# Kernel optimization log

Measured on AMD Instinct MI355X. Metric: run time of the kernel, lower is better.

## Reference

```python
import jax, jax.numpy as jnp
import numpy as np

B, S, H, E, T, L = 128, 1024, 512, 512, 64, 128


def setup_inputs() -> dict:
    key = jax.random.key(0)
    ks = jax.random.split(key, 20)
    s = 0.02
    inp = {
        "sent_lengths": jax.random.randint(ks[0], (B,), 1, S, dtype=jnp.int32),
        "output_length": T,
        "decoder_input": jax.random.normal(ks[1], (B, E), jnp.float32),
        "h0": jax.random.normal(ks[2], (B, H), jnp.float32),
        "c0": jax.random.normal(ks[3], (B, H), jnp.float32),
        "context": jax.random.normal(ks[4], (B, S, H), jnp.float32),
        "cur_labels": jax.random.randint(ks[5], (B, T), 0, L, dtype=jnp.int32),
        "cur_max_nsymbs": jax.random.randint(ks[6], (B,), 0, 10, dtype=jnp.int32),
        # parameters
        "label_emb": jax.random.normal(ks[7], (L, E), jnp.float32) * s,
        "W_ih": jax.random.normal(ks[8], (4 * H, E), jnp.float32) * s,
        "b_ih": jnp.zeros((4 * H,), jnp.float32),
        "W_hh": jax.random.normal(ks[9], (4 * H, H), jnp.float32) * s,
        "b_hh": jnp.zeros((4 * H,), jnp.float32),
        "W_ho": jax.random.normal(ks[10], (H, 2 * H), jnp.float32) * s,
        "b_ho": jnp.zeros((H,), jnp.float32),
        "W_attn_in": jax.random.normal(ks[11], (H, H), jnp.float32) * s,
        "b_attn_in": jnp.zeros((H,), jnp.float32),
        "W_attn_ctx": jax.random.normal(ks[12], (H, H), jnp.float32) * s,
        "b_attn_ctx": jnp.zeros((H,), jnp.float32),
        "V": jax.random.uniform(ks[13], (H,), jnp.float32, -1.0, 1.0),
        "W_out": jax.random.normal(ks[14], (L, 2 * H + E), jnp.float32) * s,
        "b_out": jnp.zeros((L,), jnp.float32),
    }
    # padding_idx row of the label embedding is zero (torch nn.Embedding semantics)
    inp["label_emb"] = inp["label_emb"].at[0].set(0.0)
    return inp


def _decode(output_length, decoder_input, h0, c0, context, cur_labels,
            label_emb, W_ih, b_ih, W_hh, b_hh, W_ho, b_ho,
            W_attn_in, b_attn_in, W_attn_ctx, b_attn_ctx, V, W_out, b_out):
    # Precompute the 1x1-conv context projection once (identical math to per-step conv).
    ctx = jnp.einsum("bsh,gh->bsg", context, W_attn_ctx) + b_attn_ctx  # [B,S,H]

    # Teacher-forced input sequence: x_0 = decoder_input, x_i = emb(labels[:, i-1]).
    emb = label_emb[cur_labels]                     # [B,T,E]
    xs = jnp.concatenate(
        [decoder_input[None], jnp.swapaxes(emb, 0, 1)[: output_length - 1]], axis=0
    )                                               # [T,B,E]

    def step(carry, x):
        h, c = carry
        gates = x @ W_ih.T + b_ih + h @ W_hh.T + b_hh          # [B,4H]
        i_g, f_g, g_g, o_g = jnp.split(gates, 4, axis=1)
        c_t = jax.nn.sigmoid(f_g) * c + jax.nn.sigmoid(i_g) * jnp.tanh(g_g)
        h_lstm = jax.nn.sigmoid(o_g) * jnp.tanh(c_t)            # [B,H]
        # pointer attention
        inp = h_lstm @ W_attn_in.T + b_attn_in                  # [B,H]
        att = jnp.einsum("bsh,h->bs", jnp.tanh(inp[:, None, :] + ctx), V)
        alpha = jax.nn.softmax(att, axis=-1)                    # [B,S]
        weighted = jnp.einsum("bs,bsh->bh", alpha, ctx)         # [B,H]
        hidden_t = jnp.tanh(jnp.concatenate([weighted, h_lstm], 1) @ W_ho.T + b_ho)
        out = jnp.concatenate([hidden_t, weighted, x], 1) @ W_out.T + b_out  # [B,L]
        return (hidden_t, c_t), out

    (h_f, c_f), outs = jax.lax.scan(step, (h0, c0), xs)  # outs [T,B,L]
    outputs = jnp.transpose(outs, (1, 0, 2))             # [B,T,L]
    preds = jnp.argmax(outputs, axis=-1)                 # [B,T]
    return outputs, preds, h_f, c_f


def reference(sent_lengths, output_length, decoder_input, h0, c0, context,
              cur_labels, cur_max_nsymbs, label_emb, W_ih, b_ih, W_hh, b_hh,
              W_ho, b_ho, W_attn_in, b_attn_in, W_attn_ctx, b_attn_ctx, V,
              W_out, b_out):
    # cur_batch_len = len(sent_lengths) == B, so hidden slicing is a no-op here.
    # cur_max_nsymbs unused (constrained_decoding=None path).
    return _decode(output_length, decoder_input, h0, c0, context, cur_labels,
                   label_emb, W_ih, b_ih, W_hh, b_hh, W_ho, b_ho,
                   W_attn_in, b_attn_in, W_attn_ctx, b_attn_ctx, V, W_out, b_out)
```

## Files before the change

kernel.cpp:

```cpp
#include <hip/hip_runtime.h>
#include <hip/hip_bf16.h>
#include <math.h>

#define B_ 128
#define S_ 1024
#define H_ 512
#define E_ 512
#define T_ 64
#define L_ 128
#define G4H 2048
#define QS 8

typedef __attribute__((ext_vector_type(8))) short bf16x8;
typedef __attribute__((ext_vector_type(4))) float f32x4;

__device__ inline float sigmoidf_(float x) { return 1.f / (1.f + expf(-x)); }
__device__ inline float fast_tanhf_(float x) {
    float e = __expf(2.f * x);
    return 1.f - 2.f / (e + 1.f);
}
__device__ inline unsigned f2bf1(float f) {
    unsigned u = __float_as_uint(f);
    return (u + 0x7fffu + ((u >> 16) & 1u)) >> 16;
}

#define LDP 40
__global__ __launch_bounds__(256) void gemm_split(
    const float* __restrict__ A, int lda,
    const float* __restrict__ W, int ldw,
    const float* __restrict__ bias,
    const float* __restrict__ Cinit, int ldci,
    float* __restrict__ C, int ldc,
    int K, int act, int perm)
{
    __shared__ unsigned short Ah[128 * LDP];
    __shared__ unsigned short Al[128 * LDP];
    __shared__ unsigned short Bh[128 * LDP];
    __shared__ unsigned short Bl[128 * LDP];
    const int n0 = blockIdx.x * 128;
    const int m0 = blockIdx.y * 128;
    const int t = threadIdx.x;
    const int lane = t & 63, wv = t >> 6;
    const int wr = wv >> 1, wc = wv & 1;
    const int row = t >> 1, koff = (t & 1) * 16;

    f32x4 acc[4][4] = {};

    float av[16], wvv[16];
    {
        const float* ap = A + (size_t)(m0 + row) * lda + koff;
        const float* wp = W + (size_t)(n0 + row) * ldw + koff;
#pragma unroll
        for (int q = 0; q < 4; ++q) {
            *reinterpret_cast<float4*>(&av[q * 4]) = *reinterpret_cast<const float4*>(ap + q * 4);
            *reinterpret_cast<float4*>(&wvv[q * 4]) = *reinterpret_cast<const float4*>(wp + q * 4);
        }
    }

    for (int kt = 0; kt < K; kt += 32) {
        unsigned short ah[16], al[16], bh[16], bl[16];
#pragma unroll
        for (int e = 0; e < 16; ++e) {
            unsigned ha = f2bf1(av[e]);
            float hf = __uint_as_float(ha << 16);
            ah[e] = (unsigned short)ha;
            al[e] = (unsigned short)f2bf1(av[e] - hf);
            unsigned hw = f2bf1(wvv[e]);
            float hwf = __uint_as_float(hw << 16);
            bh[e] = (unsigned short)hw;
            bl[e] = (unsigned short)f2bf1(wvv[e] - hwf);
        }
        __syncthreads();
        *reinterpret_cast<uint4*>(&Ah[row * LDP + koff])     = *reinterpret_cast<uint4*>(&ah[0]);
        *reinterpret_cast<uint4*>(&Ah[row * LDP + koff + 8]) = *reinterpret_cast<uint4*>(&ah[8]);
        *reinterpret_cast<uint4*>(&Al[row * LDP + koff])     = *reinterpret_cast<uint4*>(&al[0]);
        *reinterpret_cast<uint4*>(&Al[row * LDP + koff + 8]) = *reinterpret_cast<uint4*>(&al[8]);
        *reinterpret_cast<uint4*>(&Bh[row * LDP + koff])     = *reinterpret_cast<uint4*>(&bh[0]);
        *reinterpret_cast<uint4*>(&Bh[row * LDP + koff + 8]) = *reinterpret_cast<uint4*>(&bh[8]);
        *reinterpret_cast<uint4*>(&Bl[row * LDP + koff])     = *reinterpret_cast<uint4*>(&bl[0]);
        *reinterpret_cast<uint4*>(&Bl[row * LDP + koff + 8]) = *reinterpret_cast<uint4*>(&bl[8]);
        __syncthreads();

        if (kt + 32 < K) {
            const float* ap = A + (size_t)(m0 + row) * lda + kt + 32 + koff;
            const float* wp = W + (size_t)(n0 + row) * ldw + kt + 32 + koff;
#pragma unroll
            for (int q = 0; q < 4; ++q) {
                *reinterpret_cast<float4*>(&av[q * 4]) = *reinterpret_cast<const float4*>(ap + q * 4);
                *reinterpret_cast<float4*>(&wvv[q * 4]) = *reinterpret_cast<const float4*>(wp + q * 4);
            }
        }

        bf16x8 fah[4], fal[4], fbh[4], fbl[4];
        const int kq = (lane >> 4) * 8;
#pragma unroll
        for (int i = 0; i < 4; ++i) {
            const int ar = wr * 64 + i * 16 + (lane & 15);
            const int br = wc * 64 + i * 16 + (lane & 15);
            fah[i] = *reinterpret_cast<const bf16x8*>(&Ah[ar * LDP + kq]);
            fal[i] = *reinterpret_cast<const bf16x8*>(&Al[ar * LDP + kq]);
            fbh[i] = *reinterpret_cast<const bf16x8*>(&Bh[br * LDP + kq]);
            fbl[i] = *reinterpret_cast<const bf16x8*>(&Bl[br * LDP + kq]);
        }
#pragma unroll
        for (int i = 0; i < 4; ++i)
#pragma unroll
            for (int j = 0; j < 4; ++j) {
                acc[i][j] = __builtin_amdgcn_mfma_f32_16x16x32_bf16(fah[i], fbh[j], acc[i][j], 0, 0, 0);
                acc[i][j] = __builtin_amdgcn_mfma_f32_16x16x32_bf16(fal[i], fbh[j], acc[i][j], 0, 0, 0);
                acc[i][j] = __builtin_amdgcn_mfma_f32_16x16x32_bf16(fah[i], fbl[j], acc[i][j], 0, 0, 0);
            }
    }

#pragma unroll
    for (int i = 0; i < 4; ++i)
#pragma unroll
        for (int j = 0; j < 4; ++j) {
            const int n = n0 + wc * 64 + j * 16 + (lane & 15);
            const float bs = bias ? bias[n] : 0.f;
#pragma unroll
            for (int r = 0; r < 4; ++r) {
                const int m = m0 + wr * 64 + i * 16 + (lane >> 4) * 4 + r;
                float v = acc[i][j][r] + bs;
                if (Cinit) v += Cinit[(size_t)m * ldci + n];
                if (act == 1) v = tanhf(v);
                size_t crow;
                if (perm) { int bb = m & 127, tt = m >> 7; crow = ((size_t)bb * T_ + tt) * ldc; }
                else crow = (size_t)m * ldc;
                C[crow + n] = v;
            }
        }
}

__global__ __launch_bounds__(128) void k_perm(
    const float* __restrict__ W_ih, const float* __restrict__ W_hh,
    const float* __restrict__ b_ih, const float* __restrict__ b_hh,
    float* __restrict__ Wip, float* __restrict__ Whp, float* __restrict__ bp)
{
    int rp = blockIdx.x;
    int h = rp >> 2, g = rp & 3;
    int src = g * 512 + h;
    int t = threadIdx.x;
    const float4* si = reinterpret_cast<const float4*>(W_ih + (size_t)src * 512);
    const float4* sh = reinterpret_cast<const float4*>(W_hh + (size_t)src * 512);
    float4* di = reinterpret_cast<float4*>(Wip + (size_t)rp * 512);
    float4* dh = reinterpret_cast<float4*>(Whp + (size_t)rp * 512);
    di[t] = si[t];
    dh[t] = sh[t];
    if (t == 0) bp[rp] = b_ih[src] + b_hh[src];
}

__global__ __launch_bounds__(256) void k_gateslstm(
    const float* __restrict__ hbuf,
    const float* __restrict__ Whp,
    const float* __restrict__ xproj_t,
    float* __restrict__ cbuf,
    float* __restrict__ hlstm)
{
    __shared__ float As[16][32];
    __shared__ float Ws[16][64];
    const int n0 = blockIdx.x * 64;
    const int m0 = blockIdx.y * 32;
    const int t = threadIdx.x;
    const int tx = t & 15;
    const int ty = t >> 4;
    const int alr = t >> 3, alk = (t & 7) * 2;
    const int wlr = t >> 2, wlk = (t & 3) * 4;

    float acc[2][4] = {};

    float2 pa = *reinterpret_cast<const float2*>(hbuf + (size_t)(m0 + alr) * 512 + alk);
    float4 pv = *reinterpret_cast<const float4*>(Whp + (size_t)(n0 + wlr) * 512 + wlk);

    for (int k0 = 0; k0 < 512; k0 += 16) {
        __syncthreads();
        As[alk + 0][alr] = pa.x; As[alk + 1][alr] = pa.y;
        Ws[wlk + 0][wlr] = pv.x; Ws[wlk + 1][wlr] = pv.y;
        Ws[wlk + 2][wlr] = pv.z; Ws[wlk + 3][wlr] = pv.w;
        __syncthreads();
        if (k0 + 16 < 512) {
            pa = *reinterpret_cast<const float2*>(hbuf + (size_t)(m0 + alr) * 512 + k0 + 16 + alk);
            pv = *reinterpret_cast<const float4*>(Whp + (size_t)(n0 + wlr) * 512 + k0 + 16 + wlk);
        }
#pragma unroll
        for (int kk = 0; kk < 16; ++kk) {
            float a[2], b[4];
            a[0] = As[kk][ty * 2]; a[1] = As[kk][ty * 2 + 1];
#pragma unroll
            for (int j = 0; j < 4; ++j) b[j] = Ws[kk][tx * 4 + j];
#pragma unroll
            for (int i = 0; i < 2; ++i)
#pragma unroll
                for (int j = 0; j < 4; ++j) acc[i][j] = fmaf(a[i], b[j], acc[i][j]);
        }
    }

    const int h = (n0 >> 2) + tx;
#pragma unroll
    for (int i = 0; i < 2; ++i) {
        const int b = m0 + ty * 2 + i;
        float4 xp = *reinterpret_cast<const float4*>(xproj_t + (size_t)b * G4H + n0 + tx * 4);
        float ig = sigmoidf_(acc[i][0] + xp.x);
        float fg = sigmoidf_(acc[i][1] + xp.y);
        float gg = tanhf(acc[i][2] + xp.z);
        float og = sigmoidf_(acc[i][3] + xp.w);
        float c = fg * cbuf[(size_t)b * 512 + h] + ig * gg;
        cbuf[(size_t)b * 512 + h] = c;
        hlstm[(size_t)b * 512 + h] = og * tanhf(c);
    }
}

__global__ __launch_bounds__(256) void gemm_stepk(
    const float* __restrict__ A, int lda,
    const float* __restrict__ W, int ldw,
    float* __restrict__ P, int N, int Kc)
{
    __shared__ float As[16][128];
    __shared__ float Ws[16][64];
    const int n0 = blockIdx.x * 64;
    const int k0 = blockIdx.y * Kc;
    const int t = threadIdx.x;
    const int tx = t & 15;
    const int ty = t >> 4;
    const int ar = t >> 1, akq = (t & 1) * 8;
    const int wr = t >> 2, wkq = (t & 3) * 4;

    float acc[8][4] = {};

    float4 a0 = *reinterpret_cast<const float4*>(A + (size_t)ar * lda + k0 + akq);
    float4 a1 = *reinterpret_cast<const float4*>(A + (size_t)ar * lda + k0 + akq + 4);
    float4 w0 = *reinterpret_cast<const float4*>(W + (size_t)(n0 + wr) * ldw + k0 + wkq);

    for (int kb = 0; kb < Kc; kb += 16) {
        __syncthreads();
        As[akq + 0][ar] = a0.x; As[akq + 1][ar] = a0.y; As[akq + 2][ar] = a0.z; As[akq + 3][ar] = a0.w;
        As[akq + 4][ar] = a1.x; As[akq + 5][ar] = a1.y; As[akq + 6][ar] = a1.z; As[akq + 7][ar] = a1.w;
        Ws[wkq + 0][wr] = w0.x; Ws[wkq + 1][wr] = w0.y; Ws[wkq + 2][wr] = w0.z; Ws[wkq + 3][wr] = w0.w;
        __syncthreads();
        if (kb + 16 < Kc) {
            a0 = *reinterpret_cast<const float4*>(A + (size_t)ar * lda + k0 + kb + 16 + akq);
            a1 = *reinterpret_cast<const float4*>(A + (size_t)ar * lda + k0 + kb + 16 + akq + 4);
            w0 = *reinterpret_cast<const float4*>(W + (size_t)(n0 + wr) * ldw + k0 + kb + 16 + wkq);
        }
#pragma unroll
        for (int kk = 0; kk < 16; ++kk) {
            float a[8], b[4];
#pragma unroll
            for (int i = 0; i < 8; ++i) a[i] = As[kk][ty * 8 + i];
#pragma unroll
            for (int j = 0; j < 4; ++j) b[j] = Ws[kk][tx * 4 + j];
#pragma unroll
            for (int i = 0; i < 8; ++i)
#pragma unroll
                for (int j = 0; j < 4; ++j) acc[i][j] = fmaf(a[i], b[j], acc[i][j]);
        }
    }

#pragma unroll
    for (int i = 0; i < 8; ++i) {
        const int m = ty * 8 + i;
#pragma unroll
        for (int j = 0; j < 4; ++j)
            P[((size_t)blockIdx.y * 128 + m) * N + n0 + tx * 4 + j] = acc[i][j];
    }
}

__global__ __launch_bounds__(256) void k_who(
    const float* __restrict__ pm, const float* __restrict__ pl,
    const float* __restrict__ pw, const float* __restrict__ hlstm,
    const float* __restrict__ W_ho,
    float* __restrict__ P, float* __restrict__ hist_t)
{
    __shared__ float As[16][128];
    __shared__ float Ws[16][64];
    __shared__ float eql[128][QS];
    const int n0 = blockIdx.x * 64;
    const int k0 = blockIdx.y * 128;
    const int t = threadIdx.x;
    const int tx = t & 15;
    const int ty = t >> 4;
    const int ar = t >> 1, akq = (t & 1) * 8;
    const int wr = t >> 2, wkq = (t & 3) * 4;
    const bool merge_side = (k0 < 512);
    const bool writer = (blockIdx.x == 0) && merge_side;

    if (merge_side && t < 128) {
        float mq[QS], eq[QS];
        float M = -INFINITY;
#pragma unroll
        for (int q = 0; q < QS; ++q) { mq[q] = pm[QS * t + q]; M = fmaxf(M, mq[q]); }
        float Lt = 0.f;
#pragma unroll
        for (int q = 0; q < QS; ++q) { eq[q] = __expf(mq[q] - M); Lt += eq[q] * pl[QS * t + q]; }
        float inv = 1.f / Lt;
#pragma unroll
        for (int q = 0; q < QS; ++q) eql[t][q] = eq[q] * inv;
    }
    __syncthreads();

    float acc[8][4] = {};
    float av[8];
    float4 w0;

    auto load_stage = [&](int kb) {
        const int kg = k0 + kb + akq;
        if (merge_side) {
#pragma unroll
            for (int e = 0; e < 8; ++e) av[e] = 0.f;
#pragma unroll
            for (int q = 0; q < QS; ++q) {
                const float* pr = pw + (size_t)(QS * ar + q) * 512 + kg;
                float4 pa = *reinterpret_cast<const float4*>(pr);
                float4 pb = *reinterpret_cast<const float4*>(pr + 4);
                float qw = eql[ar][q];
                av[0] = fmaf(qw, pa.x, av[0]); av[1] = fmaf(qw, pa.y, av[1]);
                av[2] = fmaf(qw, pa.z, av[2]); av[3] = fmaf(qw, pa.w, av[3]);
                av[4] = fmaf(qw, pb.x, av[4]); av[5] = fmaf(qw, pb.y, av[5]);
                av[6] = fmaf(qw, pb.z, av[6]); av[7] = fmaf(qw, pb.w, av[7]);
            }
            if (writer) {
                *reinterpret_cast<float4*>(hist_t + (size_t)ar * 1024 + 512 + kg) = *reinterpret_cast<float4*>(&av[0]);
                *reinterpret_cast<float4*>(hist_t + (size_t)ar * 1024 + 512 + kg + 4) = *reinterpret_cast<float4*>(&av[4]);
            }
        } else {
            *reinterpret_cast<float4*>(&av[0]) = *reinterpret_cast<const float4*>(hlstm + (size_t)ar * 512 + kg - 512);
            *reinterpret_cast<float4*>(&av[4]) = *reinterpret_cast<const float4*>(hlstm + (size_t)ar * 512 + kg - 512 + 4);
        }
        w0 = *reinterpret_cast<const float4*>(W_ho + (size_t)(n0 + wr) * 1024 + k0 + kb + wkq);
    };

    load_stage(0);

    for (int kb = 0; kb < 128; kb += 16) {
        __syncthreads();
        As[akq + 0][ar] = av[0]; As[akq + 1][ar] = av[1]; As[akq + 2][ar] = av[2]; As[akq + 3][ar] = av[3];
        As[akq + 4][ar] = av[4]; As[akq + 5][ar] = av[5]; As[akq + 6][ar] = av[6]; As[akq + 7][ar] = av[7];
        Ws[wkq + 0][wr] = w0.x; Ws[wkq + 1][wr] = w0.y; Ws[wkq + 2][wr] = w0.z; Ws[wkq + 3][wr] = w0.w;
        __syncthreads();
        if (kb + 16 < 128) load_stage(kb + 16);
#pragma unroll
        for (int kk = 0; kk < 16; ++kk) {
            float a[8], b[4];
#pragma unroll
            for (int i = 0; i < 8; ++i) a[i] = As[kk][ty * 8 + i];
#pragma unroll
            for (int j = 0; j < 4; ++j) b[j] = Ws[kk][tx * 4 + j];
#pragma unroll
            for (int i = 0; i < 8; ++i)
#pragma unroll
                for (int j = 0; j < 4; ++j) acc[i][j] = fmaf(a[i], b[j], acc[i][j]);
        }
    }

#pragma unroll
    for (int i = 0; i < 8; ++i) {
        const int m = ty * 8 + i;
#pragma unroll
        for (int j = 0; j < 4; ++j)
            P[((size_t)blockIdx.y * 128 + m) * 512 + n0 + tx * 4 + j] = acc[i][j];
    }
}

__global__ void k_embed(const float* __restrict__ dec_in, const int* __restrict__ labels,
                        const float* __restrict__ emb, float* __restrict__ X)
{
    size_t total = (size_t)T_ * B_ * E_;
    for (size_t i = (size_t)blockIdx.x * blockDim.x + threadIdx.x; i < total;
         i += (size_t)gridDim.x * blockDim.x) {
        int e = (int)(i % E_);
        int b = (int)((i / E_) % B_);
        int t = (int)(i / ((size_t)E_ * B_));
        float v;
        if (t == 0) v = dec_in[b * E_ + e];
        else {
            int lab = labels[b * T_ + (t - 1)];
            v = emb[(size_t)lab * E_ + e];
        }
        X[i] = v;
    }
}

__global__ void k_init(const float* __restrict__ h0, const float* __restrict__ c0,
                       float* __restrict__ hbuf, float* __restrict__ cbuf)
{
    int i = blockIdx.x * blockDim.x + threadIdx.x;
    hbuf[i] = h0[i];
    cbuf[i] = c0[i];
}

__global__ __launch_bounds__(512) void k_attn(const float* __restrict__ ctx,
    const float* __restrict__ Pa, const float* __restrict__ b_ain,
    const float* __restrict__ Vv,
    float* __restrict__ pm, float* __restrict__ pl, float* __restrict__ pw)
{
    int blk = blockIdx.x;
    int b = blk >> 3, q = blk & 7;
    int tid = threadIdx.x, lane = tid & 63, wv = tid >> 6;

    __shared__ float inp_sh[512];
    inp_sh[tid] = Pa[(size_t)b * 512 + tid]
                + Pa[(size_t)(128 + b) * 512 + tid]
                + Pa[(size_t)(256 + b) * 512 + tid]
                + Pa[(size_t)(384 + b) * 512 + tid]
                + b_ain[tid];
    __syncthreads();

    float inpr[8], vr[8];
    {
        const float4* v4 = reinterpret_cast<const float4*>(Vv) + lane * 2;
        *(float4*)&vr[0] = v4[0];   *(float4*)&vr[4] = v4[1];
#pragma unroll
        for (int k = 0; k < 8; ++k) inpr[k] = inp_sh[lane * 8 + k];
    }
    const float* sp = ctx + ((size_t)b * S_ + q * 128 + wv * 16) * H_ + lane * 8;

    float m = -INFINITY, l = 0.f, w[8] = {};
    float4 c0 = *reinterpret_cast<const float4*>(sp);
    float4 c1 = *reinterpret_cast<const float4*>(sp + 4);
    for (int si = 0; si < 16; ++si) {
        float4 u0 = c0, u1 = c1;
        if (si < 15) {
            c0 = *reinterpret_cast<const float4*>(sp + (size_t)(si + 1) * H_);
            c1 = *reinterpret_cast<const float4*>(sp + (size_t)(si + 1) * H_ + 4);
        }
        float c8[8];
        *(float4*)&c8[0] = u0; *(float4*)&c8[4] = u1;
        float t = 0.f;
#pragma unroll
        for (int k = 0; k < 8; ++k) t = fmaf(fast_tanhf_(inpr[k] + c8[k]), vr[k], t);
#pragma unroll
        for (int off = 32; off > 0; off >>= 1) t += __shfl_xor(t, off);
        float mn = fmaxf(m, t);
        float sc = __expf(m - mn);
        float p  = __expf(t - mn);
        l = l * sc + p;
#pragma unroll
        for (int k = 0; k < 8; ++k) w[k] = w[k] * sc + p * c8[k];
        m = mn;
    }

    __shared__ float wl[8 * 512];
    __shared__ float ml[8], ll[8];
#pragma unroll
    for (int k = 0; k < 8; ++k) wl[wv * 512 + lane * 8 + k] = w[k];
    if (lane == 0) { ml[wv] = m; ll[wv] = l; }
    __syncthreads();

    float M = ml[0];
#pragma unroll
    for (int u = 1; u < 8; ++u) M = fmaxf(M, ml[u]);
    float lt = 0.f, wt = 0.f;
#pragma unroll
    for (int u = 0; u < 8; ++u) {
        float e = __expf(ml[u] - M);
        lt += e * ll[u];
        wt += e * wl[u * 512 + tid];
    }
    if (tid == 0) { pm[blk] = M; pl[blk] = lt; }
    pw[(size_t)blk * 512 + tid] = wt;
}

__global__ __launch_bounds__(256) void k_whofin(const float* __restrict__ Po,
    const float* __restrict__ b_ho, float* __restrict__ hbuf, float* __restrict__ hist_t)
{
    int i = blockIdx.x * blockDim.x + threadIdx.x;
    int b = i >> 9, h = i & 511;
    float v = b_ho[h];
#pragma unroll
    for (int ks = 0; ks < 8; ++ks) v += Po[((size_t)ks * 128 + b) * 512 + h];
    v = tanhf(v);
    hbuf[i] = v;
    hist_t[(size_t)b * 1024 + h] = v;
}

__global__ __launch_bounds__(128) void k_argmax(const float* __restrict__ outp,
                                                float* __restrict__ preds)
{
    int row = blockIdx.x;
    int tid = threadIdx.x;
    float v = outp[(size_t)row * L_ + tid];
    int idx = tid;
#pragma unroll
    for (int off = 32; off > 0; off >>= 1) {
        float ov = __shfl_xor(v, off);
        int oi = __shfl_xor(idx, off);
        if (ov > v || (ov == v && oi < idx)) { v = ov; idx = oi; }
    }
    __shared__ float sv[2];
    __shared__ int si[2];
    if ((tid & 63) == 0) { sv[tid >> 6] = v; si[tid >> 6] = idx; }
    __syncthreads();
    if (tid == 0) {
        float v0 = sv[0], v1 = sv[1];
        int i0 = si[0], i1 = si[1];
        int r = (v1 > v0 || (v1 == v0 && i1 < i0)) ? i1 : i0;
        preds[row] = (float)r;
    }
}

__global__ void k_final(const float* __restrict__ hbuf, const float* __restrict__ cbuf,
                        float* __restrict__ hf, float* __restrict__ cf)
{
    int i = blockIdx.x * blockDim.x + threadIdx.x;
    hf[i] = hbuf[i];
    cf[i] = cbuf[i];
}

extern "C" void kernel_launch(void* const* d_in, const int* in_sizes, int n_in,
                              void* d_out, int out_size, void* d_ws, size_t ws_size,
                              hipStream_t stream)
{
    const float* dec_in  = (const float*)d_in[2];
    const float* h0      = (const float*)d_in[3];
    const float* c0      = (const float*)d_in[4];
    const float* context = (const float*)d_in[5];
    const int*   labels  = (const int*)d_in[6];
    const float* emb     = (const float*)d_in[8];
    const float* W_ih    = (const float*)d_in[9];
    const float* b_ih    = (const float*)d_in[10];
    const float* W_hh    = (const float*)d_in[11];
    const float* b_hh    = (const float*)d_in[12];
    const float* W_ho    = (const float*)d_in[13];
    const float* b_ho    = (const float*)d_in[14];
    const float* W_ain   = (const float*)d_in[15];
    const float* b_ain   = (const float*)d_in[16];
    const float* W_actx  = (const float*)d_in[17];
    const float* b_actx  = (const float*)d_in[18];
    const float* Vv      = (const float*)d_in[19];
    const float* W_out   = (const float*)d_in[20];
    const float* b_out   = (const float*)d_in[21];

    float* ws = (float*)d_ws;
    float* X     = ws; ws += (size_t)T_ * B_ * E_;
    float* xproj = ws; ws += (size_t)T_ * B_ * G4H;
    float* xout  = ws; ws += (size_t)T_ * B_ * L_;
    float* ctx   = ws; ws += (size_t)B_ * S_ * H_;
    float* hist  = ws; ws += (size_t)T_ * B_ * 1024;
    float* Wip   = ws; ws += (size_t)G4H * 512;
    float* Whp   = ws; ws += (size_t)G4H * 512;
    float* bp    = ws; ws += G4H;
    float* Pa    = ws; ws += (size_t)4 * B_ * H_;
    float* Po    = ws; ws += (size_t)8 * B_ * H_;
    float* cbuf  = ws; ws += (size_t)B_ * H_;
    float* hbuf  = ws; ws += (size_t)B_ * H_;
    float* hlstm = ws; ws += (size_t)B_ * H_;
    float* pm    = ws; ws += (size_t)B_ * QS;
    float* pl    = ws; ws += (size_t)B_ * QS;
    float* pw    = ws; ws += (size_t)B_ * QS * 512;

    float* out_logits = (float*)d_out;
    float* out_preds  = out_logits + (size_t)B_ * T_ * L_;
    float* out_hf     = out_preds + (size_t)B_ * T_;
    float* out_cf     = out_hf + (size_t)B_ * H_;

    k_embed<<<2048, 256, 0, stream>>>(dec_in, labels, emb, X);
    k_init<<<256, 256, 0, stream>>>(h0, c0, hbuf, cbuf);
    k_perm<<<G4H, 128, 0, stream>>>(W_ih, W_hh, b_ih, b_hh, Wip, Whp, bp);
    gemm_split<<<dim3(16, 64), 256, 0, stream>>>(X, E_, Wip, E_, bp, nullptr, 0,
                                                 xproj, G4H, E_, 0, 0);
    gemm_split<<<dim3(1, 64), 256, 0, stream>>>(X, E_, W_out + 1024, 1536, b_out, nullptr, 0,
                                                xout, L_, E_, 0, 0);
    gemm_split<<<dim3(4, 1024), 256, 0, stream>>>(context, H_, W_actx, H_, b_actx, nullptr, 0,
                                                  ctx, H_, H_, 0, 0);

    for (int t = 0; t < T_; ++t) {
        float* hist_t = hist + (size_t)t * B_ * 1024;
        k_gateslstm<<<dim3(32, 4), 256, 0, stream>>>(hbuf, Whp,
                                                     xproj + (size_t)t * B_ * G4H,
                                                     cbuf, hlstm);
        gemm_stepk<<<dim3(8, 4), 256, 0, stream>>>(hlstm, H_, W_ain, H_, Pa, H_, 128);
        k_attn<<<B_ * QS, 512, 0, stream>>>(ctx, Pa, b_ain, Vv, pm, pl, pw);
        k_who<<<dim3(8, 8), 256, 0, stream>>>(pm, pl, pw, hlstm, W_ho, Po, hist_t);
        k_whofin<<<256, 256, 0, stream>>>(Po, b_ho, hbuf, hist_t);
    }

    gemm_split<<<dim3(1, 64), 256, 0, stream>>>(hist, 1024, W_out, 1536, nullptr,
                                                xout, L_, out_logits, L_, 1024, 0, 1);
    k_argmax<<<B_ * T_, 128, 0, stream>>>(out_logits, out_preds);
    k_final<<<256, 256, 0, stream>>>(hbuf, cbuf, out_hf, out_cf);
}
```

Before: 7.470 ms.

## Fuse W_ho split-K GEMM with tanh finalize and deepen attention context prefetch

The split-K W_ho GEMM plus its separate reduce/tanh kernel are replaced by one kernel. Each block now covers a 16-row by 64-column tile over the full K=1024, computes the attention merge on the fly, and applies bias and tanh before writing hbuf and hist. This removes one launch per decode step and the Po partial-sum buffer. In exchange each block runs a longer serial K loop with two barriers per 16-wide slice and scalar gathers. The attention kernel also prefetches four context rows ahead instead of one, to hide global load latency.

After: 10.51 ms. +40.7%, slower.

```diff
diff --git a/kernel.cpp b/kernel.cpp
--- a/kernel.cpp
+++ b/kernel.cpp
@@ -265,102 +265,6 @@
     }
 }
 
-__global__ __launch_bounds__(256) void k_who(
-    const float* __restrict__ pm, const float* __restrict__ pl,
-    const float* __restrict__ pw, const float* __restrict__ hlstm,
-    const float* __restrict__ W_ho,
-    float* __restrict__ P, float* __restrict__ hist_t)
-{
-    __shared__ float As[16][128];
-    __shared__ float Ws[16][64];
-    __shared__ float eql[128][QS];
-    const int n0 = blockIdx.x * 64;
-    const int k0 = blockIdx.y * 128;
-    const int t = threadIdx.x;
-    const int tx = t & 15;
-    const int ty = t >> 4;
-    const int ar = t >> 1, akq = (t & 1) * 8;
-    const int wr = t >> 2, wkq = (t & 3) * 4;
-    const bool merge_side = (k0 < 512);
-    const bool writer = (blockIdx.x == 0) && merge_side;
-
-    if (merge_side && t < 128) {
-        float mq[QS], eq[QS];
-        float M = -INFINITY;
-#pragma unroll
-        for (int q = 0; q < QS; ++q) { mq[q] = pm[QS * t + q]; M = fmaxf(M, mq[q]); }
-        float Lt = 0.f;
-#pragma unroll
-        for (int q = 0; q < QS; ++q) { eq[q] = __expf(mq[q] - M); Lt += eq[q] * pl[QS * t + q]; }
-        float inv = 1.f / Lt;
-#pragma unroll
-        for (int q = 0; q < QS; ++q) eql[t][q] = eq[q] * inv;
-    }
-    __syncthreads();
-
-    float acc[8][4] = {};
-    float av[8];
-    float4 w0;
-
-    auto load_stage = [&](int kb) {
-        const int kg = k0 + kb + akq;
-        if (merge_side) {
-#pragma unroll
-            for (int e = 0; e < 8; ++e) av[e] = 0.f;
-#pragma unroll
-            for (int q = 0; q < QS; ++q) {
-                const float* pr = pw + (size_t)(QS * ar + q) * 512 + kg;
-                float4 pa = *reinterpret_cast<const float4*>(pr);
-                float4 pb = *reinterpret_cast<const float4*>(pr + 4);
-                float qw = eql[ar][q];
-                av[0] = fmaf(qw, pa.x, av[0]); av[1] = fmaf(qw, pa.y, av[1]);
-                av[2] = fmaf(qw, pa.z, av[2]); av[3] = fmaf(qw, pa.w, av[3]);
-                av[4] = fmaf(qw, pb.x, av[4]); av[5] = fmaf(qw, pb.y, av[5]);
-                av[6] = fmaf(qw, pb.z, av[6]); av[7] = fmaf(qw, pb.w, av[7]);
-            }
-            if (writer) {
-                *reinterpret_cast<float4*>(hist_t + (size_t)ar * 1024 + 512 + kg) = *reinterpret_cast<float4*>(&av[0]);
-                *reinterpret_cast<float4*>(hist_t + (size_t)ar * 1024 + 512 + kg + 4) = *reinterpret_cast<float4*>(&av[4]);
-            }
-        } else {
-            *reinterpret_cast<float4*>(&av[0]) = *reinterpret_cast<const float4*>(hlstm + (size_t)ar * 512 + kg - 512);
-            *reinterpret_cast<float4*>(&av[4]) = *reinterpret_cast<const float4*>(hlstm + (size_t)ar * 512 + kg - 512 + 4);
-        }
-        w0 = *reinterpret_cast<const float4*>(W_ho + (size_t)(n0 + wr) * 1024 + k0 + kb + wkq);
-    };
-
-    load_stage(0);
-
-    for (int kb = 0; kb < 128; kb += 16) {
-        __syncthreads();
-        As[akq + 0][ar] = av[0]; As[akq + 1][ar] = av[1]; As[akq + 2][ar] = av[2]; As[akq + 3][ar] = av[3];
-        As[akq + 4][ar] = av[4]; As[akq + 5][ar] = av[5]; As[akq + 6][ar] = av[6]; As[akq + 7][ar] = av[7];
-        Ws[wkq + 0][wr] = w0.x; Ws[wkq + 1][wr] = w0.y; Ws[wkq + 2][wr] = w0.z; Ws[wkq + 3][wr] = w0.w;
-        __syncthreads();
-        if (kb + 16 < 128) load_stage(kb + 16);
-#pragma unroll
-        for (int kk = 0; kk < 16; ++kk) {
-            float a[8], b[4];
-#pragma unroll
-            for (int i = 0; i < 8; ++i) a[i] = As[kk][ty * 8 + i];
-#pragma unroll
-            for (int j = 0; j < 4; ++j) b[j] = Ws[kk][tx * 4 + j];
-#pragma unroll
-            for (int i = 0; i < 8; ++i)
-#pragma unroll
-                for (int j = 0; j < 4; ++j) acc[i][j] = fmaf(a[i], b[j], acc[i][j]);
-        }
-    }
-
-#pragma unroll
-    for (int i = 0; i < 8; ++i) {
-        const int m = ty * 8 + i;
-#pragma unroll
-        for (int j = 0; j < 4; ++j)
-            P[((size_t)blockIdx.y * 128 + m) * 512 + n0 + tx * 4 + j] = acc[i][j];
-    }
-}
-
 __global__ void k_embed(const float* __restrict__ dec_in, const int* __restrict__ labels,
                         const float* __restrict__ emb, float* __restrict__ X)
 {
@@ -415,14 +319,8 @@
     const float* sp = ctx + ((size_t)b * S_ + q * 128 + wv * 16) * H_ + lane * 8;
 
     float m = -INFINITY, l = 0.f, w[8] = {};
-    float4 c0 = *reinterpret_cast<const float4*>(sp);
-    float4 c1 = *reinterpret_cast<const float4*>(sp + 4);
-    for (int si = 0; si < 16; ++si) {
-        float4 u0 = c0, u1 = c1;
-        if (si < 15) {
-            c0 = *reinterpret_cast<const float4*>(sp + (size_t)(si + 1) * H_);
-            c1 = *reinterpret_cast<const float4*>(sp + (size_t)(si + 1) * H_ + 4);
-        }
+
+    auto process = [&](float4 u0, float4 u1) {
         float c8[8];
         *(float4*)&c8[0] = u0; *(float4*)&c8[4] = u1;
         float t = 0.f;
@@ -437,6 +335,25 @@
 #pragma unroll
         for (int k = 0; k < 8; ++k) w[k] = w[k] * sc + p * c8[k];
         m = mn;
+    };
+
+    float4 a0[4], a1[4];
+#pragma unroll
+    for (int j = 0; j < 4; ++j) {
+        a0[j] = *reinterpret_cast<const float4*>(sp + (size_t)j * H_);
+        a1[j] = *reinterpret_cast<const float4*>(sp + (size_t)j * H_ + 4);
+    }
+    for (int so = 0; so < 16; so += 4) {
+        const bool pf = (so + 4 < 16);
+#pragma unroll
+        for (int j = 0; j < 4; ++j) {
+            float4 u0 = a0[j], u1 = a1[j];
+            if (pf) {
+                a0[j] = *reinterpret_cast<const float4*>(sp + (size_t)(so + 4 + j) * H_);
+                a1[j] = *reinterpret_cast<const float4*>(sp + (size_t)(so + 4 + j) * H_ + 4);
+            }
+            process(u0, u1);
+        }
     }
 
     __shared__ float wl[8 * 512];
@@ -460,17 +377,94 @@
     pw[(size_t)blk * 512 + tid] = wt;
 }
 
-__global__ __launch_bounds__(256) void k_whofin(const float* __restrict__ Po,
-    const float* __restrict__ b_ho, float* __restrict__ hbuf, float* __restrict__ hist_t)
+__global__ __launch_bounds__(256) void k_whoF(
+    const float* __restrict__ pm, const float* __restrict__ pl,
+    const float* __restrict__ pw, const float* __restrict__ hlstm,
+    const float* __restrict__ W_ho, const float* __restrict__ b_ho,
+    const float* __restrict__ cbuf,
+    float* __restrict__ hbuf, float* __restrict__ hist_t, int last)
+{
+    __shared__ float As[16][16];
+    __shared__ float Ws[16][64];
+    __shared__ float eql[16][QS];
+    const int n0 = blockIdx.x * 64;
+    const int m0 = blockIdx.y * 16;
+    const int nt = blockIdx.x;
+    const int t0 = threadIdx.x;
+    const int ty = t0 >> 4, tx = t0 & 15;
+    const int alr = t0 & 15, alk = t0 >> 4;
+    const int wlr = t0 & 63, wk4 = (t0 >> 6) * 4;
+
+    if (t0 < 16) {
+        const int row = m0 + t0;
+        float mq[QS], eq[QS];
+        float M = -INFINITY;
+#pragma unroll
+        for (int q = 0; q < QS; ++q) { mq[q] = pm[row * QS + q]; M = fmaxf(M, mq[q]); }
+        float Lt = 0.f;
+#pragma unroll
+        for (int q = 0; q < QS; ++q) { eq[q] = __expf(mq[q] - M); Lt += eq[q] * pl[row * QS + q]; }
+        float inv = 1.f / Lt;
+#pragma unroll
+        for (int q = 0; q < QS; ++q) eql[t0][q] = eq[q] * inv;
+    }
+    __syncthreads();
+
+    float acc[4] = {};
+    auto ld_a = [&](int k0) -> float {
+        const int row = m0 + alr;
+        const int k = k0 + alk;
+        if (k0 < 512) {
+            float v = 0.f;
+#pragma unroll
+            for (int q = 0; q < QS; ++q)
+                v = fmaf(eql[alr][q], pw[((size_t)(row * QS + q)) * 512 + k], v);
+            if (nt == 0) hist_t[(size_t)row * 1024 + 512 + k] = v;
+            return v;
+        }
+        return hlstm[(size_t)row * 512 + k - 512];
+    };
+
+    float pa = ld_a(0);
+    float4 pv = *reinterpret_cast<const float4*>(W_ho + (size_t)(n0 + wlr) * 1024 + wk4);
+    for (int k0 = 0; k0 < 1024; k0 += 16) {
+        __syncthreads();
+        As[alk][alr] = pa;
+        Ws[wk4 + 0][wlr] = pv.x; Ws[wk4 + 1][wlr] = pv.y;
+        Ws[wk4 + 2][wlr] = pv.z; Ws[wk4 + 3][wlr] = pv.w;
+        __syncthreads();
+        if (k0 + 16 < 1024) {
+            pa = ld_a(k0 + 16);
+            pv = *reinterpret_cast<const float4*>(W_ho + (size_t)(n0 + wlr) * 1024 + k0 + 16 + wk4);
+        }
+#pragma unroll
+        for (int kk = 0; kk < 16; ++kk) {
+            float a = As[kk][ty];
+#pragma unroll
+            for (int j = 0; j < 4; ++j) acc[j] = fmaf(a, Ws[kk][tx * 4 + j], acc[j]);
+        }
+    }
+
+    const int b = m0 + ty;
+    float* out_hf = hbuf;
+    (void)out_hf;
+#pragma unroll
+    for (int j = 0; j < 4; ++j) {
+        const int n = n0 + tx * 4 + j;
+        float v = tanhf(acc[j] + b_ho[n]);
+        hbuf[(size_t)b * 512 + n] = v;
+        hist_t[(size_t)b * 1024 + n] = v;
+    }
+    if (last) {
+    }
+}
+
+__global__ __launch_bounds__(256) void k_fin(const float* __restrict__ hbuf,
+    const float* __restrict__ cbuf, float* __restrict__ hf, float* __restrict__ cf)
 {
     int i = blockIdx.x * blockDim.x + threadIdx.x;
-    int b = i >> 9, h = i & 511;
-    float v = b_ho[h];
-#pragma unroll
-    for (int ks = 0; ks < 8; ++ks) v += Po[((size_t)ks * 128 + b) * 512 + h];
-    v = tanhf(v);
-    hbuf[i] = v;
-    hist_t[(size_t)b * 1024 + h] = v;
+    hf[i] = hbuf[i];
+    cf[i] = cbuf[i];
 }
 
 __global__ __launch_bounds__(128) void k_argmax(const float* __restrict__ outp,
@@ -496,14 +490,6 @@
         int r = (v1 > v0 || (v1 == v0 && i1 < i0)) ? i1 : i0;
         preds[row] = (float)r;
     }
-}
-
-__global__ void k_final(const float* __restrict__ hbuf, const float* __restrict__ cbuf,
-                        float* __restrict__ hf, float* __restrict__ cf)
-{
-    int i = blockIdx.x * blockDim.x + threadIdx.x;
-    hf[i] = hbuf[i];
-    cf[i] = cbuf[i];
 }
 
 extern "C" void kernel_launch(void* const* d_in, const int* in_sizes, int n_in,
@@ -540,7 +526,6 @@
     float* Whp   = ws; ws += (size_t)G4H * 512;
     float* bp    = ws; ws += G4H;
     float* Pa    = ws; ws += (size_t)4 * B_ * H_;
-    float* Po    = ws; ws += (size_t)8 * B_ * H_;
     float* cbuf  = ws; ws += (size_t)B_ * H_;
     float* hbuf  = ws; ws += (size_t)B_ * H_;
     float* hlstm = ws; ws += (size_t)B_ * H_;
@@ -570,12 +555,12 @@
                                                      cbuf, hlstm);
         gemm_stepk<<<dim3(8, 4), 256, 0, stream>>>(hlstm, H_, W_ain, H_, Pa, H_, 128);
         k_attn<<<B_ * QS, 512, 0, stream>>>(ctx, Pa, b_ain, Vv, pm, pl, pw);
-        k_who<<<dim3(8, 8), 256, 0, stream>>>(pm, pl, pw, hlstm, W_ho, Po, hist_t);
-        k_whofin<<<256, 256, 0, stream>>>(Po, b_ho, hbuf, hist_t);
-    }
-
+        k_whoF<<<dim3(8, 8), 256, 0, stream>>>(pm, pl, pw, hlstm, W_ho, b_ho, cbuf,
+                                               hbuf, hist_t, t == T_ - 1 ? 1 : 0);
+    }
+
+    k_fin<<<256, 256, 0, stream>>>(hbuf, cbuf, out_hf, out_cf);
     gemm_split<<<dim3(1, 64), 256, 0, stream>>>(hist, 1024, W_out, 1536, nullptr,
                                                 xout, L_, out_logits, L_, 1024, 0, 1);
     k_argmax<<<B_ * T_, 128, 0, stream>>>(out_logits, out_preds);
-    k_final<<<256, 256, 0, stream>>>(hbuf, cbuf, out_hf, out_cf);
-}
+}
```
